# Optimization experiments

Hardware: AMD Instinct MI355X
Metric: run time of the kernel (lower is better)

The kernel has to match this reference:

```python
import jax, jax.numpy as jnp
from jax import lax
import numpy as np

B, T, N, HORIZON = 64, 12, 512, 12
IN_DIM = 1; OUT_DIM = 1; YCOV = 1
RNN = 64; MEM_NUM = 20; MEM_DIM = 64; EMB = 10; CHEB_K = 3
DEC_DIM = RNN + MEM_DIM  # 128


def _xavier(key, shape):
    fan_in, fan_out = shape[0], shape[-1]
    std = float(np.sqrt(2.0 / (fan_in + fan_out)))
    return jax.random.normal(key, shape, dtype=jnp.float32) * std


def _cheb_feats(A, x, batched):
    mm = (lambda a, v: jnp.einsum('bnm,bmc->bnc', a, v)) if batched else (lambda a, v: jnp.einsum('nm,bmc->bnc', a, v))
    gs = [x, mm(A, x)]
    for _ in range(CHEB_K - 2):
        gs.append(2.0 * mm(A, gs[-1]) - gs[-2])
    return jnp.concatenate(gs, axis=-1)


def _agcn(x, A, W, b, batched):
    return _cheb_feats(A, x, batched) @ W + b


def _cell(x, state, A, Wg, bg, Wu, bu, batched):
    # AGCRN GRU cell
    hid = state.shape[-1]
    inp = jnp.concatenate([x, state], axis=-1)
    z_r = jax.nn.sigmoid(_agcn(inp, A, Wg, bg, batched))
    z, r = z_r[..., :hid], z_r[..., hid:]
    cand = jnp.concatenate([x, z * state], axis=-1)
    hc = jnp.tanh(_agcn(cand, A, Wu, bu, batched))
    return r * state + (1.0 - r) * hc


def _encode(x, A, Wg, bg, Wu, bu):
    # x: [B,T,N,C] -> last hidden state [B,N,RNN]
    xt = jnp.swapaxes(x, 0, 1)  # [T,B,N,C]
    init = jnp.zeros((x.shape[0], x.shape[2], RNN), x.dtype)
    def step(state, xt_):
        h = _cell(xt_, state, A, Wg, bg, Wu, bu, batched=False)
        return h, None
    h_t, _ = lax.scan(step, init, xt)
    return h_t


def _query_memory(h_t, Memory, Wq):
    q = h_t @ Wq                                   # [B,N,mem_dim]
    att = jax.nn.softmax(q @ Memory.T, axis=-1)    # [B,N,mem_num]
    value = att @ Memory                           # [B,N,mem_dim]
    _, ind = lax.top_k(att, 2)
    pos = Memory[ind[..., 0]]                      # [B,N,mem_dim]
    return value, pos


def setup_inputs() -> dict:
    key = jax.random.key(0)
    ks = jax.random.split(key, 20)
    x = jax.random.normal(ks[0], (B, T, N, IN_DIM), dtype=jnp.float32)
    x_cov = jax.random.normal(ks[1], (B, T, N, 1), dtype=jnp.float32)
    x_his = jax.random.normal(ks[2], (B, T, N, IN_DIM), dtype=jnp.float32)
    y_cov = jax.random.normal(ks[3], (B, HORIZON, N, YCOV), dtype=jnp.float32)
    a = jax.random.uniform(ks[4], (N, N), dtype=jnp.float32)
    adj = a / jnp.sum(a, axis=-1, keepdims=True)
    enc_in = IN_DIM + RNN
    dec_in = OUT_DIM + YCOV + DEC_DIM
    return {
        'x': x, 'x_cov': x_cov, 'x_his': x_his, 'y_cov': y_cov, 'adj': adj,
        'enc_gate_W': _xavier(ks[5], (CHEB_K * enc_in, 2 * RNN)),
        'enc_gate_b': jnp.zeros((2 * RNN,), jnp.float32),
        'enc_upd_W': _xavier(ks[6], (CHEB_K * enc_in, RNN)),
        'enc_upd_b': jnp.zeros((RNN,), jnp.float32),
        'dec_gate_W': _xavier(ks[7], (CHEB_K * dec_in, 2 * DEC_DIM)),
        'dec_gate_b': jnp.zeros((2 * DEC_DIM,), jnp.float32),
        'dec_upd_W': _xavier(ks[8], (CHEB_K * dec_in, DEC_DIM)),
        'dec_upd_b': jnp.zeros((DEC_DIM,), jnp.float32),
        'Memory': _xavier(ks[9], (MEM_NUM, MEM_DIM)),
        'Wq': _xavier(ks[10], (RNN, MEM_DIM)),
        'hyper_W': _xavier(ks[11], (DEC_DIM, EMB)),
        'hyper_b': jnp.zeros((EMB,), jnp.float32),
        'lat_W': _xavier(ks[12], (MEM_DIM, 1)),
        'lat_b': jnp.zeros((1,), jnp.float32),
        'proj_W': _xavier(ks[13], (DEC_DIM, OUT_DIM)),
        'proj_b': jnp.zeros((OUT_DIM,), jnp.float32),
    }


def reference(x, x_cov, x_his, y_cov, adj,
              enc_gate_W, enc_gate_b, enc_upd_W, enc_upd_b,
              dec_gate_W, dec_gate_b, dec_upd_W, dec_upd_b,
              Memory, Wq, hyper_W, hyper_b, lat_W, lat_b, proj_W, proj_b):
    # --- encoder on x and x_his (shared weights, single static support) ---
    h_t = _encode(x, adj, enc_gate_W, enc_gate_b, enc_upd_W, enc_upd_b)
    h_att, pos = _query_memory(h_t, Memory, Wq)
    h_his_t = _encode(x_his, adj, enc_gate_W, enc_gate_b, enc_upd_W, enc_upd_b)
    _, pos_his = _query_memory(h_his_t, Memory, Wq)
    # schema==1 latent distance head (sigmoid activation)
    latent_dis = jax.nn.sigmoid(((pos - pos_his) @ lat_W + lat_b)[..., 0])  # [B,N]
    # --- adaptive decoder support from hypernetwork ---
    h_aug = jnp.concatenate([h_t, h_att], axis=-1)          # [B,N,DEC_DIM]
    node_emb = h_aug @ hyper_W + hyper_b                    # [B,N,EMB]
    support = jax.nn.softmax(jax.nn.relu(jnp.einsum('bnc,bmc->bnm', node_emb, node_emb)), axis=-1)  # [B,N,N]
    # --- decoder rollout (inference path, no teacher forcing) ---
    go0 = jnp.zeros((x.shape[0], N, OUT_DIM), x.dtype)
    ycov_t = jnp.swapaxes(y_cov, 0, 1)  # [HORIZON,B,N,YCOV]
    def dec_step(carry, yc):
        go, h = carry
        xt = jnp.concatenate([go, yc], axis=-1)
        h = _cell(xt, h, support, dec_gate_W, dec_gate_b, dec_upd_W, dec_upd_b, batched=True)
        go = h @ proj_W + proj_b
        return (go, h), go
    _, outs = lax.scan(dec_step, (go0, h_aug), ycov_t)
    output = jnp.swapaxes(outs, 0, 1)  # [B,HORIZON,N,OUT_DIM]
    return output, latent_dis
```

## Files before the change

kernel.cpp:

```cpp
#include <hip/hip_runtime.h>
#include <hip/hip_bf16.h>


typedef __attribute__((ext_vector_type(8))) short s8v;
typedef __attribute__((ext_vector_type(4))) float f4v;
typedef __attribute__((ext_vector_type(4))) unsigned short u4v;

__device__ __forceinline__ float b2f(unsigned short u){
  union{unsigned int i; float f;} v; v.i = ((unsigned int)u)<<16; return v.f;
}
__device__ __forceinline__ unsigned short f2b(float f){
  union{float f; unsigned int i;} v; v.f = f;
  unsigned int r = v.i + 0x7fff + ((v.i >> 16) & 1);
  return (unsigned short)(r >> 16);
}

__global__ void k_zero16(uint4* p, int n){
  int i = blockIdx.x*256 + threadIdx.x;
  if (i < n) p[i] = make_uint4(0,0,0,0);
}


__global__ void k_reorderF(const float* __restrict__ W, float* __restrict__ Wr,
                           int HC, int NEX, int SEGW, int J){
  int idx = blockIdx.x*256 + threadIdx.x;
  int K = 3*SEGW;
  if (idx >= K*J) return;
  int k = idx / J, j = idx - k*J;
  int seg = k / SEGW, c = k - seg*SEGW;
  int CIN = HC + NEX;
  float v = 0.f;
  if (c < HC)       v = W[(size_t)(seg*CIN + NEX + c)*J + j];
  else if (c < CIN) v = W[(size_t)(seg*CIN + (c-HC))*J + j];
  Wr[(size_t)k*J + j] = v;
}

__global__ __launch_bounds__(256) void k_a2e(const float* __restrict__ A,
                                             float* __restrict__ A2e){
  __shared__ __align__(16) float As[32][132];
  __shared__ __align__(16) float Bs[32][132];
  int t = threadIdx.x;
  int r0 = (blockIdx.x & 3) * 128;
  int c0 = (blockIdx.x >> 2) * 128;
  int tr = t & 15, tc = t >> 4;
  float acc[8][8];
  #pragma unroll
  for (int i=0;i<8;i++)
    #pragma unroll
    for (int j=0;j<8;j++) acc[i][j]=0.f;
  for (int k0=0;k0<512;k0+=32){
    #pragma unroll
    for (int i=0;i<4;i++){
      int s = t + i*256;
      int k = s & 31, rq = s >> 5;
      const float* ap = A + (size_t)(r0 + rq*4)*512 + k0 + k;
      float4 v;
      v.x = ap[0]; v.y = ap[512]; v.z = ap[1024]; v.w = ap[1536];
      *(float4*)&As[k][rq*4] = v;
    }
    #pragma unroll
    for (int i=0;i<4;i++){
      int s = t + i*256;
      int k = s >> 5, cq = s & 31;
      float4 v = *(const float4*)(A + (size_t)(k0+k)*512 + c0 + cq*4);
      *(float4*)&Bs[k][cq*4] = v;
    }
    __syncthreads();
    #pragma unroll 8
    for (int k=0;k<32;k++){
      float a[8], b[8];
      *(float4*)&a[0] = *(const float4*)&As[k][tr*4];
      *(float4*)&a[4] = *(const float4*)&As[k][64+tr*4];
      *(float4*)&b[0] = *(const float4*)&Bs[k][tc*4];
      *(float4*)&b[4] = *(const float4*)&Bs[k][64+tc*4];
      #pragma unroll
      for (int i=0;i<8;i++)
        #pragma unroll
        for (int j=0;j<8;j++) acc[i][j] += a[i]*b[j];
    }
    __syncthreads();
  }
  #pragma unroll
  for (int i=0;i<8;i++){
    int r = r0 + (i<4 ? tr*4+i : 64+tr*4+i-4);
    #pragma unroll
    for (int j=0;j<8;j++){
      int c = c0 + (j<4 ? tc*4+j : 64+tc*4+j-4);
      A2e[(size_t)r*512 + c] = 2.f*acc[i][j] - (r==c ? 1.f : 0.f);
    }
  }
}

template<int MODE>
__global__ __launch_bounds__(256) void k_enc(
    const float* __restrict__ A, const float* __restrict__ A2e,
    const float* __restrict__ hsrc,
    const float* __restrict__ xa, const float* __restrict__ xb,
    int tstep, const float* __restrict__ Wr, const float* __restrict__ bias,
    float* __restrict__ zh, float* __restrict__ rbuf, float* __restrict__ henc)
{
  constexpr int J  = (MODE==0) ? 128 : 64;
  constexpr int TN = (MODE==0) ? 8 : 4;
  __shared__ __align__(16) float R1[4352];
  __shared__ __align__(16) float F0t[65][66];
  float (*sA)[68]   = (float(*)[68])(R1);
  float (*sA2)[68]  = (float(*)[68])(R1 + 1088);
  float (*sB)[68]   = (float(*)[68])(R1 + 2176);
  float (*G12h)[66] = (float(*)[66])(R1);
  const int t = threadIdx.x;
  const int bb = blockIdx.x;
  const int rowblk = blockIdx.z;
  const int n0 = rowblk * 64;
  const int tr = t & 15, tc = t >> 4;
  const int xrow = t & 63, xmat = (t >> 6) & 1;
  const float* xp = (bb < 64) ? (xa + ((size_t)bb*12 + tstep)*512)
                              : (xb + ((size_t)(bb-64)*12 + tstep)*512);

  float acc[2][4][4];
  #pragma unroll
  for (int m=0;m<2;m++)
    #pragma unroll
    for (int i=0;i<4;i++)
      #pragma unroll
      for (int j=0;j<4;j++) acc[m][i][j]=0.f;
  float xacc = 0.f;

  for (int k0=0;k0<512;k0+=16){
    {
      int k = t & 15, rq = t >> 4;
      const float* ap  = A   + (size_t)(n0 + rq*4)*512 + k0 + k;
      const float* a2p = A2e + (size_t)(n0 + rq*4)*512 + k0 + k;
      float4 v, w;
      v.x = ap[0];  v.y = ap[512];  v.z = ap[1024];  v.w = ap[1536];
      w.x = a2p[0]; w.y = a2p[512]; w.z = a2p[1024]; w.w = a2p[1536];
      *(float4*)&sA[k][rq*4]  = v;
      *(float4*)&sA2[k][rq*4] = w;
    }
    {
      int k = t >> 4, cq = t & 15;
      *(float4*)&sB[k][cq*4] = *(const float4*)(hsrc + (size_t)(bb*512 + k0 + k)*64 + cq*4);
    }
    if (t < 16) sB[t][64] = xp[k0 + t];
    __syncthreads();
    #pragma unroll 4
    for (int k=0;k<16;k++){
      float a1[4], a2[4], b[4];
      *(float4*)&a1[0] = *(const float4*)&sA[k][tr*4];
      *(float4*)&a2[0] = *(const float4*)&sA2[k][tr*4];
      *(float4*)&b[0]  = *(const float4*)&sB[k][tc*4];
      #pragma unroll
      for (int i=0;i<4;i++)
        #pragma unroll
        for (int j=0;j<4;j++){
          acc[0][i][j] += a1[i]*b[j];
          acc[1][i][j] += a2[i]*b[j];
        }
      float am = xmat ? sA2[k][xrow] : sA[k][xrow];
      xacc += am * sB[k][64];
    }
    if ((k0 >> 6) == rowblk){
      const int off = k0 & 63;
      for (int s=t; s<1040; s+=256){
        int c = s >> 4, kk = s & 15;
        F0t[c][off + kk] = sB[kk][c];
      }
    }
    __syncthreads();
  }

  #pragma unroll
  for (int j=0;j<4;j++){
    float4 v;
    v.x = acc[0][0][j]; v.y = acc[0][1][j];
    v.z = acc[0][2][j]; v.w = acc[0][3][j];
    *(float4*)&G12h[tc*4 + j][tr*4] = v;
  }
  if (t < 64) G12h[64][xrow] = xacc;
  __syncthreads();

  float acc2[4][TN];
  #pragma unroll
  for (int i=0;i<4;i++)
    #pragma unroll
    for (int jj=0;jj<TN;jj++) acc2[i][jj]=0.f;
  const int j0 = tc*TN;

  #pragma unroll 4
  for (int c=0;c<65;c++){
    float a[4], w[TN];
    *(float4*)&a[0] = *(const float4*)&F0t[c][tr*4];
    #pragma unroll
    for (int q=0;q<TN;q+=4) *(float4*)&w[q] = *(const float4*)(Wr + (size_t)c*J + j0 + q);
    #pragma unroll
    for (int i=0;i<4;i++)
      #pragma unroll
      for (int jj=0;jj<TN;jj++) acc2[i][jj] += a[i]*w[jj];
  }
  #pragma unroll 4
  for (int c=0;c<65;c++){
    float a[4], w[TN];
    *(float4*)&a[0] = *(const float4*)&G12h[c][tr*4];
    #pragma unroll
    for (int q=0;q<TN;q+=4) *(float4*)&w[q] = *(const float4*)(Wr + (size_t)(68+c)*J + j0 + q);
    #pragma unroll
    for (int i=0;i<4;i++)
      #pragma unroll
      for (int jj=0;jj<TN;jj++) acc2[i][jj] += a[i]*w[jj];
  }
  __syncthreads();
  #pragma unroll
  for (int j=0;j<4;j++){
    float4 v;
    v.x = acc[1][0][j]; v.y = acc[1][1][j];
    v.z = acc[1][2][j]; v.w = acc[1][3][j];
    *(float4*)&G12h[tc*4 + j][tr*4] = v;
  }
  if (t >= 64 && t < 128) G12h[64][xrow] = xacc;
  __syncthreads();
  #pragma unroll 4
  for (int c=0;c<65;c++){
    float a[4], w[TN];
    *(float4*)&a[0] = *(const float4*)&G12h[c][tr*4];
    #pragma unroll
    for (int q=0;q<TN;q+=4) *(float4*)&w[q] = *(const float4*)(Wr + (size_t)(136+c)*J + j0 + q);
    #pragma unroll
    for (int i=0;i<4;i++)
      #pragma unroll
      for (int jj=0;jj<TN;jj++) acc2[i][jj] += a[i]*w[jj];
  }

  float bj[TN];
  #pragma unroll
  for (int jj=0;jj<TN;jj++) bj[jj] = bias[j0+jj];
  const int gbase = bb*512 + n0;
  #pragma unroll
  for (int i=0;i<4;i++){
    const int lr = tr*4 + i;
    const int row = gbase + lr;
    if (MODE == 0){
      float s[8];
      #pragma unroll
      for (int jj=0;jj<TN;jj++) s[jj] = 1.f/(1.f + __expf(-(acc2[i][jj] + bj[jj])));
      if (j0 < 64){
        float4 o0, o1;
        o0.x = s[0]*F0t[j0+0][lr]; o0.y = s[1]*F0t[j0+1][lr];
        o0.z = s[2]*F0t[j0+2][lr]; o0.w = s[3]*F0t[j0+3][lr];
        o1.x = s[4]*F0t[j0+4][lr]; o1.y = s[5]*F0t[j0+5][lr];
        o1.z = s[6]*F0t[j0+6][lr]; o1.w = s[7]*F0t[j0+7][lr];
        *(float4*)(zh + (size_t)row*64 + j0)     = o0;
        *(float4*)(zh + (size_t)row*64 + j0 + 4) = o1;
      } else {
        float4 o0, o1;
        o0.x=s[0]; o0.y=s[1]; o0.z=s[2]; o0.w=s[3];
        o1.x=s[4]; o1.y=s[5]; o1.z=s[6]; o1.w=s[7];
        *(float4*)(rbuf + (size_t)row*64 + j0 - 64) = o0;
        *(float4*)(rbuf + (size_t)row*64 + j0 - 60) = o1;
      }
    } else {
      float4 h4 = *(const float4*)(henc + (size_t)row*64 + j0);
      float4 r4 = *(const float4*)(rbuf + (size_t)row*64 + j0);
      float hv[4] = {h4.x,h4.y,h4.z,h4.w};
      float rv[4] = {r4.x,r4.y,r4.z,r4.w};
      float ov[4];
      #pragma unroll
      for (int jj=0;jj<4;jj++){
        float hc = 1.f - 2.f/(__expf(2.f*(acc2[i][jj] + bj[jj])) + 1.f);
        ov[jj] = rv[jj]*hv[jj] + (1.f - rv[jj])*hc;
      }
      float4 o; o.x=ov[0]; o.y=ov[1]; o.z=ov[2]; o.w=ov[3];
      *(float4*)(henc + (size_t)row*64 + j0) = o;
    }
  }
}


__global__ void k_reorderB(const float* __restrict__ W, unsigned short* __restrict__ Wr,
                           int HC, int NEX, int C, int KP, int J){
  int idx = blockIdx.x*256 + threadIdx.x;
  if (idx >= J*KP) return;
  int j = idx / KP, kp = idx - j*KP;
  float v = 0.f;
  if (kp < 3*C){
    int seg = kp / C, c = kp - seg*C;
    int CIN = HC + NEX;
    if (c < HC)       v = W[(size_t)(seg*CIN + NEX + c)*J + j];
    else if (c < CIN) v = W[(size_t)(seg*CIN + (c-HC))*J + j];
  }
  Wr[(size_t)j*KP + kp] = f2b(v);
}

__global__ __launch_bounds__(256) void k_sup2(const unsigned short* __restrict__ S,
                                              unsigned short* __restrict__ S2){
  __shared__ unsigned short Bs[128*40];
  const int t = threadIdx.x;
  const int w = t >> 6, L = t & 63, lm = L & 15, q = L >> 4;
  const int bb = blockIdx.z;
  const int n0 = blockIdx.x * 128;
  const int m0 = blockIdx.y * 128;
  const unsigned short* Sb = S + (size_t)bb * 262144;
  unsigned short* S2b = S2 + (size_t)bb * 262144;
  f4v acc[2][8];
  #pragma unroll
  for (int i=0;i<2;i++)
    #pragma unroll
    for (int j=0;j<8;j++)
      #pragma unroll
      for (int r=0;r<4;r++) acc[i][j][r] = 0.f;
  for (int k0=0;k0<512;k0+=32){
    #pragma unroll
    for (int i=0;i<2;i++){
      int s = t + i*256;
      int kk = s >> 4, mg = s & 15;
      s8v v = *(const s8v*)(Sb + (size_t)(k0+kk)*512 + m0 + mg*8);
      #pragma unroll
      for (int e=0;e<8;e++) Bs[(mg*8+e)*40 + kk] = ((unsigned short*)&v)[e];
    }
    __syncthreads();
    s8v a0 = *(const s8v*)(Sb + (size_t)(n0 + w*32 + lm)*512 + k0 + q*8);
    s8v a1 = *(const s8v*)(Sb + (size_t)(n0 + w*32 + 16 + lm)*512 + k0 + q*8);
    #pragma unroll
    for (int ct=0;ct<8;ct++){
      s8v b = *(const s8v*)&Bs[(ct*16+lm)*40 + q*8];
      acc[0][ct] = __builtin_amdgcn_mfma_f32_16x16x32_bf16(a0, b, acc[0][ct], 0,0,0);
      acc[1][ct] = __builtin_amdgcn_mfma_f32_16x16x32_bf16(a1, b, acc[1][ct], 0,0,0);
    }
    __syncthreads();
  }
  #pragma unroll
  for (int rt=0;rt<2;rt++){
    const int row = n0 + w*32 + rt*16 + q*4;
    #pragma unroll
    for (int ct=0;ct<8;ct++){
      const int col = m0 + ct*16 + lm;
      #pragma unroll
      for (int r=0;r<4;r++){
        float v = 2.f*acc[rt][ct][r] - ((row+r)==col ? 1.f : 0.f);
        S2b[(size_t)(row+r)*512 + col] = f2b(v);
      }
    }
  }
}

__global__ __launch_bounds__(256) void k_mmB2(
    const unsigned short* __restrict__ M1, const unsigned short* __restrict__ M2,
    unsigned short* fC, unsigned short* fR)
{
  constexpr int C = 144;
  __shared__ unsigned short Bs[C*40];
  const int t = threadIdx.x;
  const int w = t >> 6, L = t & 63, lm = L & 15, q = L >> 4;
  const int bb = blockIdx.z;
  const int n0 = blockIdx.x * 64;
  const unsigned short* M1b = M1 + (size_t)bb * 262144;
  const unsigned short* M2b = M2 + (size_t)bb * 262144;
  unsigned short* fCb = fC + (size_t)bb * 432 * 512;
  const unsigned short* Xb = fCb;
  unsigned short* O1 = fCb + (size_t)C * 512;
  unsigned short* O2 = fCb + (size_t)2 * C * 512;
  const int rw = n0 + w*16;

  f4v acc[2][9];
  #pragma unroll
  for (int i=0;i<2;i++)
    #pragma unroll
    for (int j=0;j<9;j++)
      #pragma unroll
      for (int r=0;r<4;r++) acc[i][j][r] = 0.f;

  s8v breg[3];
  const size_t ar = (size_t)(rw + lm)*512 + q*8;
  #pragma unroll
  for (int i=0;i<3;i++){
    int s = t + i*256;
    if (s < C*4) breg[i] = *(const s8v*)(Xb + (size_t)(s>>2)*512 + (s&3)*8);
  }
  s8v a1 = *(const s8v*)(M1b + ar);
  s8v a2 = *(const s8v*)(M2b + ar);

  for (int ks=0; ks<16; ks++){
    #pragma unroll
    for (int i=0;i<3;i++){
      int s = t + i*256;
      if (s < C*4) *(s8v*)&Bs[(s>>2)*40 + (s&3)*8] = breg[i];
    }
    __syncthreads();
    const int kn = (ks < 15) ? (ks+1)*32 : 0;
    #pragma unroll
    for (int i=0;i<3;i++){
      int s = t + i*256;
      if (s < C*4) breg[i] = *(const s8v*)(Xb + (size_t)(s>>2)*512 + kn + (s&3)*8);
    }
    s8v a1n = *(const s8v*)(M1b + ar + kn);
    s8v a2n = *(const s8v*)(M2b + ar + kn);
    #pragma unroll
    for (int ct=0; ct<9; ct++){
      s8v b = *(const s8v*)&Bs[(ct*16+lm)*40 + q*8];
      acc[0][ct] = __builtin_amdgcn_mfma_f32_16x16x32_bf16(a1, b, acc[0][ct], 0,0,0);
      acc[1][ct] = __builtin_amdgcn_mfma_f32_16x16x32_bf16(a2, b, acc[1][ct], 0,0,0);
    }
    __syncthreads();
    a1 = a1n; a2 = a2n;
  }
  const int m0 = rw + q*4;
  #pragma unroll
  for (int ct=0; ct<9; ct++){
    const int c = ct*16 + lm;
    u4v o1, o2;
    #pragma unroll
    for (int r=0;r<4;r++){ o1[r] = f2b(acc[0][ct][r]); o2[r] = f2b(acc[1][ct][r]); }
    *(u4v*)(O1 + (size_t)c*512 + m0) = o1;
    *(u4v*)(O2 + (size_t)c*512 + m0) = o2;
    const size_t rb = (size_t)(bb*512 + m0)*448;
    #pragma unroll
    for (int r=0;r<4;r++){
      fR[rb + (size_t)r*448 + 144 + c] = o1[r];
      fR[rb + (size_t)r*448 + 288 + c] = o2[r];
    }
  }
}

template<int KSTEPS, int JT16, int MODE, int HC>
__global__ __launch_bounds__(256) void k_gwB(
    unsigned short* fR, int KP,
    const unsigned short* __restrict__ Wr, const float* __restrict__ bias,
    unsigned short* fC, int C3,
    float* hC, float* rbuf)
{
  constexpr int JT = JT16*16;
  constexpr int BIT = JT*4/256;
  __shared__ unsigned short Bs[JT*40];
  const int t = threadIdx.x;
  const int w = t >> 6, L = t & 63, lm = L & 15, q = L >> 4;
  const int row0 = blockIdx.x * 128;
  const int j0 = blockIdx.y * JT;
  const int rw = row0 + w*32;

  f4v acc[2][JT16];
  #pragma unroll
  for (int i=0;i<2;i++)
    #pragma unroll
    for (int j=0;j<JT16;j++)
      #pragma unroll
      for (int r=0;r<4;r++) acc[i][j][r] = 0.f;

  s8v breg[BIT];
  const unsigned short* Wb = Wr + (size_t)j0*KP;
  const size_t ar0 = (size_t)(rw + lm)*KP + q*8;
  const size_t ar1 = (size_t)(rw + 16 + lm)*KP + q*8;

  #pragma unroll
  for (int i=0;i<BIT;i++){
    int s = t + i*256;
    breg[i] = *(const s8v*)(Wb + (size_t)(s>>2)*KP + (s&3)*8);
  }
  s8v a0 = *(const s8v*)(fR + ar0);
  s8v a1 = *(const s8v*)(fR + ar1);

  for (int ks=0; ks<KSTEPS; ks++){
    #pragma unroll
    for (int i=0;i<BIT;i++){
      int s = t + i*256;
      *(s8v*)&Bs[(s>>2)*40 + (s&3)*8] = breg[i];
    }
    __syncthreads();
    const int kn = (ks < KSTEPS-1) ? (ks+1)*32 : 0;
    #pragma unroll
    for (int i=0;i<BIT;i++){
      int s = t + i*256;
      breg[i] = *(const s8v*)(Wb + (size_t)(s>>2)*KP + kn + (s&3)*8);
    }
    s8v a0n = *(const s8v*)(fR + ar0 + kn);
    s8v a1n = *(const s8v*)(fR + ar1 + kn);
    #pragma unroll
    for (int ct=0; ct<JT16; ct++){
      s8v b = *(const s8v*)&Bs[(ct*16+lm)*40 + q*8];
      acc[0][ct] = __builtin_amdgcn_mfma_f32_16x16x32_bf16(a0, b, acc[0][ct], 0,0,0);
      acc[1][ct] = __builtin_amdgcn_mfma_f32_16x16x32_bf16(a1, b, acc[1][ct], 0,0,0);
    }
    __syncthreads();
    a0 = a0n; a1 = a1n;
  }
  #pragma unroll
  for (int rt=0; rt<2; rt++){
    const int m0 = rw + rt*16 + q*4;
    const int bb = m0 >> 9, n = m0 & 511;
    #pragma unroll
    for (int ct=0; ct<JT16; ct++){
      const int j = j0 + ct*16 + lm;
      const float bj = bias[j];
      if (MODE == 0){
        if (j < HC){
          f4v h4 = *(const f4v*)(hC + ((size_t)bb*HC + j)*512 + n);
          u4v o;
          #pragma unroll
          for (int r=0;r<4;r++){
            float s = 1.f/(1.f + __expf(-(acc[rt][ct][r] + bj)));
            float zh = s * h4[r];
            o[r] = f2b(zh);
            fR[(size_t)(m0+r)*KP + j] = o[r];
          }
          *(u4v*)(fC + ((size_t)bb*C3 + j)*512 + n) = o;
        } else {
          f4v rv;
          #pragma unroll
          for (int r=0;r<4;r++) rv[r] = 1.f/(1.f + __expf(-(acc[rt][ct][r] + bj)));
          *(f4v*)(rbuf + ((size_t)bb*HC + (j-HC))*512 + n) = rv;
        }
      } else {
        f4v h4 = *(const f4v*)(hC + ((size_t)bb*HC + j)*512 + n);
        f4v r4 = *(const f4v*)(rbuf + ((size_t)bb*HC + j)*512 + n);
        u4v o; f4v hn;
        #pragma unroll
        for (int r=0;r<4;r++){
          float e = __expf(2.f*(acc[rt][ct][r] + bj));
          float hc_ = 1.f - 2.f/(e + 1.f);
          hn[r] = r4[r]*h4[r] + (1.f - r4[r])*hc_;
          o[r] = f2b(hn[r]);
          fR[(size_t)(m0+r)*KP + j] = o[r];
        }
        *(f4v*)(hC + ((size_t)bb*HC + j)*512 + n) = hn;
        *(u4v*)(fC + ((size_t)bb*C3 + j)*512 + n) = o;
      }
    }
  }
}


__global__ void k_extras_dec(const float* __restrict__ yc,
    unsigned short* fR, unsigned short* fC, int tstep){
  int rr = blockIdx.x*256 + threadIdx.x;
  int bb = rr >> 9, n = rr & 511;
  unsigned short u = f2b(yc[((size_t)bb*12 + tstep)*512 + n]);
  fR[(size_t)rr*448 + 129] = u;
  fC[((size_t)bb*432 + 129)*512 + n] = u;
}
__global__ void k_fix_go(unsigned short* fR, unsigned short* fC){
  int rr = blockIdx.x*256 + threadIdx.x;
  int bb = rr >> 9, n = rr & 511;
  fR[(size_t)rr*448 + 128] = 0;
  fC[((size_t)bb*432 + 128)*512 + n] = 0;
}

__global__ __launch_bounds__(256) void k_query(const float* __restrict__ hR,
      const float* __restrict__ Wq, const float* __restrict__ Mem,
      float* __restrict__ hCd, unsigned short* fR, unsigned short* fC,
      int* __restrict__ it, int* __restrict__ ih){
  int sub = threadIdx.x >> 6, lane = threadIdx.x & 63;
  int row = blockIdx.x*4 + sub;
  __shared__ float sh[4][64], sq[4][64], ss[4][20];
  float hv = hR[(size_t)row*64 + lane];
  sh[sub][lane] = hv;
  __syncthreads();
  float qv = 0.f;
  for (int c=0;c<64;c++) qv += sh[sub][c]*Wq[c*64 + lane];
  sq[sub][lane] = qv;
  __syncthreads();
  if (lane < 20){
    float s = 0.f;
    for (int j=0;j<64;j++) s += sq[sub][j]*Mem[lane*64 + j];
    ss[sub][lane] = s;
  }
  __syncthreads();
  float mx = -1e30f; int am = 0;
  for (int m=0;m<20;m++){ float s = ss[sub][m]; if (s > mx){ mx = s; am = m; } }
  float sum = 0.f;
  for (int m=0;m<20;m++) sum += __expf(ss[sub][m]-mx);
  float inv = 1.f/sum;
  float v = 0.f;
  for (int m=0;m<20;m++) v += __expf(ss[sub][m]-mx)*inv*Mem[m*64 + lane];
  int bb = row >> 9, n = row & 511;
  if (bb < 64){
    hCd[((size_t)bb*128 + lane)*512 + n] = hv;
    hCd[((size_t)bb*128 + 64 + lane)*512 + n] = v;
    fR[(size_t)row*448 + lane] = f2b(hv);
    fR[(size_t)row*448 + 64 + lane] = f2b(v);
    fC[((size_t)bb*432 + lane)*512 + n] = f2b(hv);
    fC[((size_t)bb*432 + 64 + lane)*512 + n] = f2b(v);
    if (lane==0) it[row] = am;
  } else {
    if (lane==0) ih[row - 32768] = am;
  }
}

__global__ void k_latent(const int* __restrict__ it, const int* __restrict__ ih,
                         const float* __restrict__ Mem,
                         const float* __restrict__ lW, const float* __restrict__ lb,
                         float* __restrict__ outl){
  int row = blockIdx.x*256 + threadIdx.x;
  int i1 = it[row], i2 = ih[row];
  float a = lb[0];
  for (int c=0;c<64;c++) a += (Mem[i1*64+c]-Mem[i2*64+c])*lW[c];
  outl[row] = 1.f/(1.f + __expf(-a));
}

__global__ __launch_bounds__(256) void k_emb(const float* __restrict__ hCd,
    const float* __restrict__ hW, const float* __restrict__ hb, float* __restrict__ emb){
  __shared__ float sW[1280];
  int t = threadIdx.x;
  for (int s=t; s<1280; s+=256) sW[s] = hW[s];
  __syncthreads();
  int rr = blockIdx.x*256 + t;
  int bb = rr >> 9, n = rr & 511;
  float a[10];
  #pragma unroll
  for (int e=0;e<10;e++) a[e] = hb[e];
  for (int c=0;c<128;c++){
    float v = hCd[((size_t)bb*128 + c)*512 + n];
    #pragma unroll
    for (int e=0;e<10;e++) a[e] += v*sW[c*10+e];
  }
  #pragma unroll
  for (int e=0;e<10;e++) emb[(size_t)rr*10 + e] = a[e];
}

__global__ __launch_bounds__(256) void k_support(const float* __restrict__ emb,
                                                 unsigned short* __restrict__ sup){
  int b = blockIdx.x >> 9;
  int n = blockIdx.x & 511;
  int t = threadIdx.x;
  __shared__ float se[5120];
  __shared__ float red[8];
  for (int s = t; s < 5120; s += 256) se[s] = emb[(size_t)b*5120 + s];
  __syncthreads();
  float en[10];
  #pragma unroll
  for (int i=0;i<10;i++) en[i] = se[n*10+i];
  float s0=0.f, s1=0.f;
  #pragma unroll
  for (int i=0;i<10;i++){ s0 += en[i]*se[t*10+i]; s1 += en[i]*se[(t+256)*10+i]; }
  s0 = fmaxf(s0, 0.f); s1 = fmaxf(s1, 0.f);
  float mx = fmaxf(s0, s1);
  for (int o=32;o>0;o>>=1) mx = fmaxf(mx, __shfl_down(mx, o));
  if ((t&63)==0) red[t>>6] = mx;
  __syncthreads();
  mx = fmaxf(fmaxf(red[0],red[1]), fmaxf(red[2],red[3]));
  float e0 = __expf(s0-mx), e1 = __expf(s1-mx);
  float sm = e0 + e1;
  for (int o=32;o>0;o>>=1) sm += __shfl_down(sm, o);
  if ((t&63)==0) red[4+(t>>6)] = sm;
  __syncthreads();
  sm = red[4]+red[5]+red[6]+red[7];
  float inv = 1.f/sm;
  size_t base = ((size_t)b*512 + n)*512;
  sup[base + t]       = f2b(e0*inv);
  sup[base + t + 256] = f2b(e1*inv);
}

__global__ __launch_bounds__(256) void k_proj(const float* __restrict__ hCd,
    const float* __restrict__ pW, const float* __restrict__ pb,
    unsigned short* fR, unsigned short* fC, float* __restrict__ out, int tstep){
  __shared__ float sW[128];
  int t = threadIdx.x;
  if (t < 128) sW[t] = pW[t];
  __syncthreads();
  int rr = blockIdx.x*256 + t;
  int bb = rr >> 9, n = rr & 511;
  float a = pb[0];
  for (int c=0;c<128;c++) a += hCd[((size_t)bb*128 + c)*512 + n]*sW[c];
  out[((size_t)bb*12 + tstep)*512 + n] = a;
  unsigned short u = f2b(a);
  fR[(size_t)rr*448 + 128] = u;
  fC[((size_t)bb*432 + 128)*512 + n] = u;
}

extern "C" void kernel_launch(void* const* d_in, const int* in_sizes, int n_in,
                              void* d_out, int out_size, void* d_ws, size_t ws_size,
                              hipStream_t stream) {
  const float* x     = (const float*)d_in[0];
  const float* x_his = (const float*)d_in[2];
  const float* y_cov = (const float*)d_in[3];
  const float* adj   = (const float*)d_in[4];
  const float* egW   = (const float*)d_in[5];
  const float* egb   = (const float*)d_in[6];
  const float* euW   = (const float*)d_in[7];
  const float* eub   = (const float*)d_in[8];
  const float* dgW   = (const float*)d_in[9];
  const float* dgb   = (const float*)d_in[10];
  const float* duW   = (const float*)d_in[11];
  const float* dub   = (const float*)d_in[12];
  const float* Mem   = (const float*)d_in[13];
  const float* Wq    = (const float*)d_in[14];
  const float* hW    = (const float*)d_in[15];
  const float* hb    = (const float*)d_in[16];
  const float* lW    = (const float*)d_in[17];
  const float* lb    = (const float*)d_in[18];
  const float* pW    = (const float*)d_in[19];
  const float* pb    = (const float*)d_in[20];
  float* out  = (float*)d_out;
  float* outl = out + 393216;

  char* base = (char*)d_ws;
  size_t off = 0;
  auto alloc = [&](size_t bytes)->char*{
    char* p = base + off; off = (off + bytes + 255) & ~(size_t)255; return p;
  };
  unsigned short* sup  = (unsigned short*)alloc(33554432);
  unsigned short* sup2 = (unsigned short*)alloc(33554432);
  float* emb  = (float*)alloc(1310720);
  int*   it   = (int*)alloc(131072);
  int*   ih   = (int*)alloc(131072);
  float* henc = (float*)alloc(16777216);
  float* zhF  = (float*)alloc(16777216);
  float* hCd  = zhF;
  float* rbF  = (float*)alloc(16777216);
  unsigned short* fR = (unsigned short*)alloc(29360128);
  unsigned short* fC = (unsigned short*)alloc(28311552);
  float* a2e = (float*)alloc(1048576);
  float* wr_egF = (float*)alloc(104448);
  float* wr_euF = (float*)alloc(52224);
  unsigned short* wr_dg = (unsigned short*)alloc(229376);
  unsigned short* wr_du = (unsigned short*)alloc(114688);
  if (ws_size < off) return;

  k_zero16<<<4096,256,0,stream>>>((uint4*)henc, 1048576);
  k_zero16<<<7168,256,0,stream>>>((uint4*)fR, 1835008);
  k_zero16<<<6912,256,0,stream>>>((uint4*)fC, 1769472);
  k_a2e<<<16,256,0,stream>>>(adj, a2e);
  k_reorderF<<<102,256,0,stream>>>(egW, wr_egF, 64,1,68,128);
  k_reorderF<<< 51,256,0,stream>>>(euW, wr_euF, 64,1,68,64);
  k_reorderB<<<448,256,0,stream>>>(dgW, wr_dg, 128,2,144,448,256);
  k_reorderB<<<224,256,0,stream>>>(duW, wr_du, 128,2,144,448,128);

  for (int t = 0; t < 12; t++){
    k_enc<0><<<dim3(128,1,8),256,0,stream>>>(adj, a2e, henc, x, x_his, t,
                                             wr_egF, egb, zhF, rbF, nullptr);
    k_enc<1><<<dim3(128,1,8),256,0,stream>>>(adj, a2e, zhF, x, x_his, t,
                                             wr_euF, eub, nullptr, rbF, henc);
  }

  k_query<<<16384,256,0,stream>>>(henc, Wq, Mem, hCd, fR, fC, it, ih);
  k_latent<<<128,256,0,stream>>>(it, ih, Mem, lW, lb, outl);
  k_emb<<<128,256,0,stream>>>(hCd, hW, hb, emb);
  k_support<<<32768,256,0,stream>>>(emb, sup);
  k_sup2<<<dim3(4,4,64),256,0,stream>>>(sup, sup2);
  k_fix_go<<<128,256,0,stream>>>(fR, fC);

  for (int t = 0; t < 12; t++){
    k_extras_dec<<<128,256,0,stream>>>(y_cov, fR, fC, t);
    k_mmB2<<<dim3(8,1,64),256,0,stream>>>(sup, sup2, fC, fR);
    k_gwB<14,16,0,128><<<dim3(256,1),256,0,stream>>>(fR, 448, wr_dg, dgb, fC, 432, hCd, rbF);
    k_mmB2<<<dim3(8,1,64),256,0,stream>>>(sup, sup2, fC, fR);
    k_gwB<14,8,1,128><<<dim3(256,1),256,0,stream>>>(fR, 448, wr_du, dub, fC, 432, hCd, rbF);
    k_proj<<<128,256,0,stream>>>(hCd, pW, pb, fR, fC, out, t);
  }
}
```

Measured before the change: 6.169 ms.

## Coalesce query writes via shared-memory transpose and split decoder gate GEMMs over grid

The query kernel now writes the augmented hidden state row-major, and a new tiled transpose kernel produces the column-major fp32 and bf16 copies through shared memory. This replaces the strided scattered stores that were there before. Separately, the decoder gate and update GEMM launches halve a template tile parameter and double the grid's y dimension to raise parallelism. The cost is an extra launch plus a staging buffer that reuses rbF.

```diff
diff --git a/kernel.cpp b/kernel.cpp
--- a/kernel.cpp
+++ b/kernel.cpp
@@ -543,7 +543,7 @@
 
 __global__ __launch_bounds__(256) void k_query(const float* __restrict__ hR,
       const float* __restrict__ Wq, const float* __restrict__ Mem,
-      float* __restrict__ hCd, unsigned short* fR, unsigned short* fC,
+      float* __restrict__ haugR, unsigned short* fR,
       int* __restrict__ it, int* __restrict__ ih){
   int sub = threadIdx.x >> 6, lane = threadIdx.x & 63;
   int row = blockIdx.x*4 + sub;
@@ -568,17 +568,39 @@
   float inv = 1.f/sum;
   float v = 0.f;
   for (int m=0;m<20;m++) v += __expf(ss[sub][m]-mx)*inv*Mem[m*64 + lane];
-  int bb = row >> 9, n = row & 511;
+  int bb = row >> 9;
   if (bb < 64){
-    hCd[((size_t)bb*128 + lane)*512 + n] = hv;
-    hCd[((size_t)bb*128 + 64 + lane)*512 + n] = v;
-    fR[(size_t)row*448 + lane] = f2b(hv);
+    haugR[(size_t)row*128 + lane]      = hv;
+    haugR[(size_t)row*128 + 64 + lane] = v;
+    fR[(size_t)row*448 + lane]      = f2b(hv);
     fR[(size_t)row*448 + 64 + lane] = f2b(v);
-    fC[((size_t)bb*432 + lane)*512 + n] = f2b(hv);
-    fC[((size_t)bb*432 + 64 + lane)*512 + n] = f2b(v);
     if (lane==0) it[row] = am;
   } else {
     if (lane==0) ih[row - 32768] = am;
+  }
+}
+
+__global__ __launch_bounds__(256) void k_tr(const float* __restrict__ haugR,
+      float* __restrict__ hCd, unsigned short* fC){
+  __shared__ float T[64][65];
+  const int t = threadIdx.x;
+  const int n0 = blockIdx.x * 64;
+  const int c0 = blockIdx.y * 64;
+  const int bb = blockIdx.z;
+  #pragma unroll
+  for (int i=0;i<16;i++){
+    int idx = t + i*256;
+    int nl = idx >> 6, cl = idx & 63;
+    T[cl][nl] = haugR[(size_t)(bb*512 + n0 + nl)*128 + c0 + cl];
+  }
+  __syncthreads();
+  #pragma unroll
+  for (int i=0;i<16;i++){
+    int idx = t + i*256;
+    int cl = idx >> 6, nl = idx & 63;
+    float v = T[cl][nl];
+    hCd[((size_t)bb*128 + c0 + cl)*512 + n0 + nl] = v;
+    fC[((size_t)bb*432 + c0 + cl)*512 + n0 + nl] = f2b(v);
   }
 }
 
@@ -703,6 +725,7 @@
   float* zhF  = (float*)alloc(16777216);
   float* hCd  = zhF;
   float* rbF  = (float*)alloc(16777216);
+  float* haugR = rbF;
   unsigned short* fR = (unsigned short*)alloc(29360128);
   unsigned short* fC = (unsigned short*)alloc(28311552);
   float* a2e = (float*)alloc(1048576);
@@ -728,7 +751,8 @@
                                              wr_euF, eub, nullptr, rbF, henc);
   }
 
-  k_query<<<16384,256,0,stream>>>(henc, Wq, Mem, hCd, fR, fC, it, ih);
+  k_query<<<16384,256,0,stream>>>(henc, Wq, Mem, haugR, fR, it, ih);
+  k_tr<<<dim3(8,2,64),256,0,stream>>>(haugR, hCd, fC);
   k_latent<<<128,256,0,stream>>>(it, ih, Mem, lW, lb, outl);
   k_emb<<<128,256,0,stream>>>(hCd, hW, hb, emb);
   k_support<<<32768,256,0,stream>>>(emb, sup);
@@ -738,9 +762,9 @@
   for (int t = 0; t < 12; t++){
     k_extras_dec<<<128,256,0,stream>>>(y_cov, fR, fC, t);
     k_mmB2<<<dim3(8,1,64),256,0,stream>>>(sup, sup2, fC, fR);
-    k_gwB<14,16,0,128><<<dim3(256,1),256,0,stream>>>(fR, 448, wr_dg, dgb, fC, 432, hCd, rbF);
+    k_gwB<14,8,0,128><<<dim3(256,2),256,0,stream>>>(fR, 448, wr_dg, dgb, fC, 432, hCd, rbF);
     k_mmB2<<<dim3(8,1,64),256,0,stream>>>(sup, sup2, fC, fR);
-    k_gwB<14,8,1,128><<<dim3(256,1),256,0,stream>>>(fR, 448, wr_du, dub, fC, 432, hCd, rbF);
+    k_gwB<14,4,1,128><<<dim3(256,2),256,0,stream>>>(fR, 448, wr_du, dub, fC, 432, hCd, rbF);
     k_proj<<<128,256,0,stream>>>(hCd, pW, pb, fR, fC, out, t);
   }
 }
```

After: 6.023 ms (median of 2 runs). -2.4%, faster.
